# Kernel tuning notes

Hardware: AMD Instinct MI355X
Metric: run time of the kernel (lower is better)

The kernel has to match this reference:

```python
import jax, jax.numpy as jnp
import numpy as np
from jax import lax

V, H, B, S, T = 32000, 512, 32, 256, 16  # vocab, hidden, batch, src_len, keyword_len


def setup_inputs() -> dict:
    key = jax.random.key(0)
    ks = jax.random.split(key, 26)
    sc = 0.02
    def P(k, *shape):
        return jax.random.normal(k, shape, jnp.float32) * sc
    return {
        "theme": jax.random.randint(ks[0], (1, B), 0, V),
        "keyword": jax.random.randint(ks[1], (T, B), 0, V),
        "src": jax.random.randint(ks[2], (S, B), 0, V),
        "theme_tab": P(ks[3], V, H),
        "keyword_tab": P(ks[4], V, H),
        "src_tab": P(ks[5], V, H),
        # GRU params (PyTorch layout: W_ih/W_hh are (3H, H) stacked r,z,n)
        "Wih_f": P(ks[6], 3 * H, H), "Whh_f": P(ks[7], 3 * H, H),
        "bih_f": P(ks[8], 3 * H), "bhh_f": P(ks[9], 3 * H),
        "Wih_b": P(ks[10], 3 * H, H), "Whh_b": P(ks[11], 3 * H, H),
        "bih_b": P(ks[12], 3 * H), "bhh_b": P(ks[13], 3 * H),
        # Linear layers (PyTorch layout: W is (out, in))
        "Ww": P(ks[14], H, 2 * H), "bw": P(ks[15], H),      # enc_w_weight
        "Wt": P(ks[16], H, H), "bt": P(ks[17], H),          # enc_theme_weight
        "Wk": P(ks[18], H, H), "bk": P(ks[19], H),          # enc_keyword_weight
        "wv": P(ks[20], H), "bv": P(ks[21]),                # enc_weight (H -> 1)
        "Wo": P(ks[22], H, 3 * H), "bo": P(ks[23], H),      # enc_output_out
        "Who": P(ks[24], H, 2 * H),                         # enc_hidden_out (no bias)
    }


def _gru_dir(x, Wih, Whh, bih, bhh, reverse):
    # x: (S, B, H). Returns (outputs (S,B,H), final hidden (B,H)).
    h = Whh.shape[1]
    gx = jnp.einsum('sbh,gh->sbg', x, Wih) + bih  # precompute input gates for all steps
    if reverse:
        gx = gx[::-1]
    h0 = jnp.zeros((x.shape[1], h), x.dtype)

    def step(hprev, g):
        gh = hprev @ Whh.T + bhh
        xr, xz, xn = jnp.split(g, 3, axis=-1)
        hr, hz, hn = jnp.split(gh, 3, axis=-1)
        r = jax.nn.sigmoid(xr + hr)
        z = jax.nn.sigmoid(xz + hz)
        n = jnp.tanh(xn + r * hn)
        hnew = (1.0 - z) * n + z * hprev
        return hnew, hnew

    hT, ys = lax.scan(step, h0, gx)
    if reverse:
        ys = ys[::-1]
    return ys, hT


def _forward(theme, keyword, src,
             theme_tab, keyword_tab, src_tab,
             Wih_f, Whh_f, bih_f, bhh_f,
             Wih_b, Whh_b, bih_b, bhh_b,
             Ww, bw, Wt, bt, Wk, bk, wv, bv, Wo, bo, Who):
    hdim = Whh_f.shape[1]
    src_emb = src_tab[src]          # (S, B, H)
    theme_emb = theme_tab[theme]    # (1, B, H)
    keyword_emb = keyword_tab[keyword]  # (T, B, H)

    ys_f, hT_f = _gru_dir(src_emb, Wih_f, Whh_f, bih_f, bhh_f, reverse=False)
    ys_b, hT_b = _gru_dir(src_emb, Wih_b, Whh_b, bih_b, bhh_b, reverse=True)
    enc_output = jnp.concatenate([ys_f, ys_b], axis=-1)   # (S, B, 2H); == enc_w_1 (the split/cat is identity)
    enc_hidden = jnp.concatenate([hT_f, hT_b], axis=-1)[None]  # (1, B, 2H)

    enc_w_1 = enc_output.transpose(1, 0, 2)     # (B, S, 2H)
    enc_theme = theme_emb.transpose(1, 0, 2)    # (B, 1, H)
    enc_keyword = keyword_emb.transpose(1, 0, 2)  # (B, T, H)

    # point(): additive-attention broadcast scoring
    b1 = enc_w_1 @ Ww.T + bw                    # (B, S, H)
    theme_proj = enc_theme[:, 0, :] @ Wt.T + bt  # (B, H)  == b22
    b3 = enc_keyword @ Wk.T + bk                # (B, T, H)
    b4 = jnp.tanh(b1[:, :, None, :] + theme_proj[:, None, None, :] + b3[:, None, :, :])  # (B,S,T,H)
    scores = b4 @ wv + bv                        # (B, S, T)
    enc_w_2 = jnp.einsum('bst,bh->bsh', scores, theme_proj)  # bmm(scores, b22 broadcast over T)

    concat_enc_w = jnp.concatenate([enc_w_2, enc_w_1], axis=-1)  # (B, S, 3H)
    enc_out = (concat_enc_w @ Wo.T + bo).transpose(1, 0, 2)      # (S, B, H)
    enc_hidden_out = enc_hidden @ Who.T                          # (1, B, H)
    return enc_out, enc_hidden_out


def reference(theme, keyword, src,
              theme_tab, keyword_tab, src_tab,
              Wih_f, Whh_f, bih_f, bhh_f,
              Wih_b, Whh_b, bih_b, bhh_b,
              Ww, bw, Wt, bt, Wk, bk, wv, bv, Wo, bo, Who):
    return _forward(theme, keyword, src,
                    theme_tab, keyword_tab, src_tab,
                    Wih_f, Whh_f, bih_f, bhh_f,
                    Wih_b, Whh_b, bih_b, bhh_b,
                    Ww, bw, Wt, bt, Wk, bk, wv, bv, Wo, bo, Who)
```

## Files before the change

### kernel.cpp

```cpp
#include <hip/hip_runtime.h>

typedef unsigned short u16;
typedef __attribute__((ext_vector_type(8))) short bf16x8;
typedef __attribute__((ext_vector_type(4))) float f32x4;

__device__ __forceinline__ float bf2f(u16 u) {
  union { unsigned int i; float f; } v; v.i = ((unsigned int)u) << 16; return v.f;
}
__device__ __forceinline__ u16 f2bf(float f) {
  union { float f; unsigned int i; } v; v.f = f;
  unsigned int r = (v.i + 0x7FFFu + ((v.i >> 16) & 1u)) >> 16;
  return (u16)r;
}
__device__ __forceinline__ float sigmoidf_(float x) { return 1.f / (1.f + __expf(-x)); }
__device__ __forceinline__ float tanhf_(float x) {
  x = fminf(fmaxf(x, -10.f), 10.f);
  float e2 = __expf(2.f * x);
  return (e2 - 1.f) / (e2 + 1.f);
}

static const size_t OFF_GX    = 0;
static const size_t OFF_HBUF  = 50331648;
static const size_t OFF_ASRC  = 67174400;
static const size_t OFF_EW1   = 75563008;
static const size_t OFF_B1    = 92340224;
static const size_t OFF_WIHC  = 109117440;
static const size_t OFF_WWB   = 112263168;
static const size_t OFF_WO2B  = 113311744;
static const size_t OFF_WKB   = 114360320;
static const size_t OFF_KWE   = 114884608;
static const size_t OFF_B3    = 115408896;
static const size_t OFF_TP    = 116457472;
static const size_t OFF_TPO   = 116523008;
static const size_t OFF_SSUM  = 116588544;
static const size_t OFF_BIASC = 116621312;
static const size_t OFF_CNT   = 116633600;

__global__ __launch_bounds__(256) void cvtk(const float* __restrict__ s,
                                            u16* __restrict__ d, int n) {
  int i = (blockIdx.x * 256 + threadIdx.x) * 4;
  if (i < n) {
    float4 v = *(const float4*)(s + i);
    ushort4 o; o.x = f2bf(v.x); o.y = f2bf(v.y); o.z = f2bf(v.z); o.w = f2bf(v.w);
    *(ushort4*)(d + i) = o;
  }
}

__global__ __launch_bounds__(256) void cvt_wo2(const float* __restrict__ Wo,
                                               u16* __restrict__ d) {
  int i = (blockIdx.x * 256 + threadIdx.x) * 4;
  int nrow = i >> 10, c = i & 1023;
  float4 v = *(const float4*)(Wo + (size_t)nrow * 1536 + 512 + c);
  ushort4 o; o.x = f2bf(v.x); o.y = f2bf(v.y); o.z = f2bf(v.z); o.w = f2bf(v.w);
  *(ushort4*)(d + i) = o;
}

__global__ __launch_bounds__(256) void gather_rows(const int* __restrict__ ids,
                                                   const float* __restrict__ tab,
                                                   u16* __restrict__ dst, int mode) {
  int i = (blockIdx.x * 256 + threadIdx.x) * 8;
  int r = i >> 9, c = i & 511;
  int id = (mode == 0) ? ids[r] : ids[((r & 15) << 5) + (r >> 4)];
  const float* s = tab + (size_t)id * 512 + c;
  alignas(16) u16 o[8];
#pragma unroll
  for (int j = 0; j < 8; ++j) o[j] = f2bf(s[j]);
  *(uint4*)(dst + i) = *(const uint4*)o;
}

__global__ __launch_bounds__(256) void proj_tp(const int* __restrict__ theme,
                                               const float* __restrict__ tab,
                                               const float* __restrict__ W,
                                               const float* __restrict__ bias,
                                               float* __restrict__ outp) {
  int o = blockIdx.x * 256 + threadIdx.x;
  int b = o >> 9, n = o & 511;
  const float* emb = tab + (size_t)theme[b] * 512;
  const float* wr = W + (size_t)n * 512;
  float acc = 0.f;
  for (int h = 0; h < 512; h += 4) {
    float4 e = *(const float4*)(emb + h);
    float4 w = *(const float4*)(wr + h);
    acc += e.x * w.x + e.y * w.y + e.z * w.z + e.w * w.w;
  }
  outp[o] = acc + bias[n];
}

__global__ __launch_bounds__(256) void proj_tpo(const float* __restrict__ tp,
                                                const float* __restrict__ Wo,
                                                float* __restrict__ outp) {
  int o = blockIdx.x * 256 + threadIdx.x;
  int b = o >> 9, n = o & 511;
  const float* emb = tp + (size_t)b * 512;
  const float* wr = Wo + (size_t)n * 1536;
  float acc = 0.f;
  for (int h = 0; h < 512; h += 4) {
    float4 e = *(const float4*)(emb + h);
    float4 w = *(const float4*)(wr + h);
    acc += e.x * w.x + e.y * w.y + e.z * w.z + e.w * w.w;
  }
  outp[o] = acc;
}

template <int EPI>
__global__ __launch_bounds__(256) void gemm_bt(const u16* __restrict__ A,
                                               const u16* __restrict__ B,
                                               const float* __restrict__ bias,
                                               float* __restrict__ Cf,
                                               u16* __restrict__ Cb, int M, int N,
                                               int K, const float* __restrict__ ssum,
                                               const float* __restrict__ tpo) {
  __shared__ u16 As[128][72];
  __shared__ u16 Bs[128][72];
  const int tid = threadIdx.x;
  const int mtiles = M >> 7;
  const int mt = blockIdx.x % mtiles, nt = blockIdx.x / mtiles;
  const int wave = tid >> 6, lane = tid & 63;
  const int wr = wave >> 1, wc = wave & 1;
  const int l16 = lane & 15, l4 = lane >> 4;
  f32x4 acc[4][4] = {};
  const int nkt = K >> 6;
  for (int kt = 0; kt < nkt; ++kt) {
    __syncthreads();
#pragma unroll
    for (int i = 0; i < 4; ++i) {
      int c = i * 256 + tid;
      int row = c >> 3, c8 = c & 7;
      uint4 va = *(const uint4*)(A + (size_t)(mt * 128 + row) * K + kt * 64 + c8 * 8);
      *(uint4*)&As[row][c8 * 8] = va;
      uint4 vb = *(const uint4*)(B + (size_t)(nt * 128 + row) * K + kt * 64 + c8 * 8);
      *(uint4*)&Bs[row][c8 * 8] = vb;
    }
    __syncthreads();
#pragma unroll
    for (int kk = 0; kk < 2; ++kk) {
      bf16x8 af[4], bfr[4];
#pragma unroll
      for (int m = 0; m < 4; ++m)
        af[m] = *(const bf16x8*)&As[wr * 64 + m * 16 + l16][kk * 32 + l4 * 8];
#pragma unroll
      for (int n = 0; n < 4; ++n)
        bfr[n] = *(const bf16x8*)&Bs[wc * 64 + n * 16 + l16][kk * 32 + l4 * 8];
#pragma unroll
      for (int m = 0; m < 4; ++m)
#pragma unroll
        for (int n = 0; n < 4; ++n)
          acc[m][n] = __builtin_amdgcn_mfma_f32_16x16x32_bf16(af[m], bfr[n],
                                                              acc[m][n], 0, 0, 0);
    }
  }
#pragma unroll
  for (int m = 0; m < 4; ++m) {
    int rg = mt * 128 + wr * 64 + m * 16 + l4 * 4;
#pragma unroll
    for (int n = 0; n < 4; ++n) {
      int cg = nt * 128 + wc * 64 + n * 16 + l16;
      float bb = bias[cg];
#pragma unroll
      for (int i = 0; i < 4; ++i) {
        int r = rg + i;
        float v = acc[m][n][i] + bb;
        if (EPI == 2) v += ssum[r] * tpo[(r & 31) * 512 + cg];
        if (EPI == 0) Cb[(size_t)r * N + cg] = f2bf(v);
        else Cf[(size_t)r * N + cg] = v;
      }
    }
  }
}

__global__ __launch_bounds__(256) void gru_scan(const u16* __restrict__ gx,
                                                const float* __restrict__ Whh_f,
                                                const float* __restrict__ Whh_b,
                                                const float* __restrict__ bhh_f,
                                                const float* __restrict__ bhh_b,
                                                u16* __restrict__ hbuf,
                                                int* __restrict__ cnt)
{
  __shared__ u16 Wl[96][520];
  __shared__ u16 hl[32 * 512];
  __shared__ float gh[32][100];
  __shared__ float hF[32][32];
  __shared__ float bhs[96];
  const int tid = threadIdx.x;
  const int bid = blockIdx.x;
  const int r8 = bid & 7;
  const int d = r8 >> 2;
  const int slice = (bid >> 3) * 4 + (r8 & 3);
  const float* Whh = d ? Whh_b : Whh_f;
  const float* bhh = d ? bhh_b : bhh_f;

  for (int e = tid * 4; e < 96 * 512; e += 1024) {
    int lr = e >> 9, c = e & 511;
    int grow = (lr >> 5) * 512 + slice * 32 + (lr & 31);
    float4 v = *(const float4*)(Whh + (size_t)grow * 512 + c);
    ushort4 o; o.x = f2bf(v.x); o.y = f2bf(v.y); o.z = f2bf(v.z); o.w = f2bf(v.w);
    *(ushort4*)&Wl[lr][c] = o;
  }
  if (tid < 96) {
    int grow = (tid >> 5) * 512 + slice * 32 + (tid & 31);
    bhs[tid] = bhh[grow];
  }
  for (int e = tid; e < 32 * 32; e += 256) hF[e >> 5][e & 31] = 0.f;

  const int wave = tid >> 6, lane = tid & 63;
  const int l16 = lane & 15, l4 = lane >> 4;
  const int mt = wave & 1, nt3 = (wave >> 1) * 3;
  const int arow = mt * 16 + l16;
  const int asw = (arow & 7) << 4;
  int* cntd = cnt + d * 257;

  __syncthreads();

  for (int t = 0; t < 256; ++t) {
    int trow = (d == 0) ? t : 255 - t;
    const u16* gxr = gx + (size_t)trow * 32 * 3072 + d * 1536 + slice * 32;
    float xr[4], xz[4], xn[4];
#pragma unroll
    for (int it = 0; it < 4; ++it) {
      int item = it * 256 + tid;
      int b = item >> 5, j = item & 31;
      const u16* gxb = gxr + (size_t)b * 3072;
      xr[it] = bf2f(gxb[j]);
      xz[it] = bf2f(gxb[512 + j]);
      xn[it] = bf2f(gxb[1024 + j]);
    }
    if (t > 0) {
      if (tid == 0) {
        while (__hip_atomic_load(cntd + t, __ATOMIC_ACQUIRE,
                                 __HIP_MEMORY_SCOPE_AGENT) < 16)
          __builtin_amdgcn_s_sleep(1);
      }
      __syncthreads();
    }
    const u16* hsrc = hbuf + ((size_t)(d * 257 + t) * 32) * 512;
#pragma unroll
    for (int i = 0; i < 8; ++i) {
      int idx = i * 256 + tid;
      int row = idx >> 6, cb = idx & 63;
      uint4 v = *(const uint4*)(hsrc + row * 512 + cb * 8);
      *(uint4*)((char*)hl + row * 1024 + ((cb * 16) ^ ((row & 7) << 4))) = v;
    }
    __syncthreads();
    f32x4 a0 = {}, a1 = {}, a2 = {};
    const char* hlb = (const char*)hl;
#pragma unroll
    for (int k = 0; k < 16; ++k) {
      int abyte = arow * 1024 + (((k * 32 + l4 * 8) * 2) ^ asw);
      bf16x8 av = *(const bf16x8*)(hlb + abyte);
      bf16x8 b0 = *(const bf16x8*)&Wl[(nt3 + 0) * 16 + l16][k * 32 + l4 * 8];
      bf16x8 b1v = *(const bf16x8*)&Wl[(nt3 + 1) * 16 + l16][k * 32 + l4 * 8];
      bf16x8 b2 = *(const bf16x8*)&Wl[(nt3 + 2) * 16 + l16][k * 32 + l4 * 8];
      a0 = __builtin_amdgcn_mfma_f32_16x16x32_bf16(av, b0, a0, 0, 0, 0);
      a1 = __builtin_amdgcn_mfma_f32_16x16x32_bf16(av, b1v, a1, 0, 0, 0);
      a2 = __builtin_amdgcn_mfma_f32_16x16x32_bf16(av, b2, a2, 0, 0, 0);
    }
    {
      int crow = mt * 16 + l4 * 4;
#pragma unroll
      for (int i = 0; i < 4; ++i) {
        gh[crow + i][(nt3 + 0) * 16 + l16] = a0[i];
        gh[crow + i][(nt3 + 1) * 16 + l16] = a1[i];
        gh[crow + i][(nt3 + 2) * 16 + l16] = a2[i];
      }
    }
    __syncthreads();
    u16* hdst = hbuf + ((size_t)(d * 257 + t + 1) * 32) * 512 + slice * 32;
#pragma unroll
    for (int it = 0; it < 4; ++it) {
      int item = it * 256 + tid;
      int b = item >> 5, j = item & 31;
      float hr = gh[b][j] + bhs[j];
      float hz = gh[b][32 + j] + bhs[32 + j];
      float hn = gh[b][64 + j] + bhs[64 + j];
      float rr = sigmoidf_(xr[it] + hr);
      float zz = sigmoidf_(xz[it] + hz);
      float nn = tanhf_(xn[it] + rr * hn);
      float hp = hF[b][j];
      float hnew = (1.f - zz) * nn + zz * hp;
      hF[b][j] = hnew;
      hdst[(size_t)b * 512 + j] = f2bf(hnew);
    }
    __syncthreads();
    if (tid == 0)
      __hip_atomic_fetch_add(cntd + t + 1, 1, __ATOMIC_RELEASE,
                             __HIP_MEMORY_SCOPE_AGENT);
  }
}

__global__ __launch_bounds__(256) void build_encw1(const u16* __restrict__ hbuf,
                                                   u16* __restrict__ ew) {
  int idx = (blockIdx.x * 256 + threadIdx.x) * 8;
  int r = idx >> 10, c = idx & 1023;
  int s = r >> 5, b = r & 31;
  size_t src;
  if (c < 512) src = ((size_t)(s + 1) * 32 + b) * 512 + c;
  else src = ((size_t)(257 + 256 - s) * 32 + b) * 512 + (c - 512);
  *(uint4*)(ew + idx) = *(const uint4*)(hbuf + src);
}

__global__ __launch_bounds__(256) void scores_k(const float* __restrict__ b1,
                                                const float* __restrict__ tp,
                                                const float* __restrict__ b3,
                                                const float* __restrict__ wv,
                                                const float* __restrict__ bv,
                                                float* __restrict__ ssum) {
  __shared__ float pre[512];
  __shared__ float wvs[512];
  __shared__ float red[4];
  int r = blockIdx.x;
  int tid = threadIdx.x;
  int b = r & 31;
  for (int h = tid; h < 512; h += 256) {
    pre[h] = b1[(size_t)r * 512 + h] + tp[b * 512 + h];
    wvs[h] = wv[h];
  }
  __syncthreads();
  float acc = 0.f;
  for (int t = 0; t < 16; ++t) {
    const float* b3r = b3 + ((size_t)b * 16 + t) * 512;
    for (int h = tid; h < 512; h += 256) acc += wvs[h] * tanhf_(pre[h] + b3r[h]);
  }
  for (int o = 32; o > 0; o >>= 1) acc += __shfl_down(acc, o);
  if ((tid & 63) == 0) red[tid >> 6] = acc;
  __syncthreads();
  if (tid == 0) ssum[r] = red[0] + red[1] + red[2] + red[3] + 16.f * bv[0];
}

__global__ __launch_bounds__(256) void hidden_k(const u16* __restrict__ hbuf,
                                                const float* __restrict__ Who,
                                                float* __restrict__ outp) {
  int o = blockIdx.x * 256 + threadIdx.x;
  int b = o >> 9, n = o & 511;
  const u16* hf = hbuf + ((size_t)256 * 32 + b) * 512;
  const u16* hb = hbuf + ((size_t)(257 + 256) * 32 + b) * 512;
  const float* w = Who + (size_t)n * 1024;
  float acc = 0.f;
  for (int k = 0; k < 512; ++k) acc += bf2f(hf[k]) * w[k];
  for (int k = 0; k < 512; ++k) acc += bf2f(hb[k]) * w[512 + k];
  outp[o] = acc;
}

extern "C" void kernel_launch(void* const* d_in, const int* in_sizes, int n_in,
                              void* d_out, int out_size, void* d_ws, size_t ws_size,
                              hipStream_t stream) {
  (void)in_sizes; (void)n_in; (void)out_size; (void)ws_size;
  const int* theme = (const int*)d_in[0];
  const int* keyword = (const int*)d_in[1];
  const int* src = (const int*)d_in[2];
  const float* theme_tab = (const float*)d_in[3];
  const float* keyword_tab = (const float*)d_in[4];
  const float* src_tab = (const float*)d_in[5];
  const float* Wih_f = (const float*)d_in[6];
  const float* Whh_f = (const float*)d_in[7];
  const float* bih_f = (const float*)d_in[8];
  const float* bhh_f = (const float*)d_in[9];
  const float* Wih_b = (const float*)d_in[10];
  const float* Whh_b = (const float*)d_in[11];
  const float* bih_b = (const float*)d_in[12];
  const float* bhh_b = (const float*)d_in[13];
  const float* Ww = (const float*)d_in[14];
  const float* bw = (const float*)d_in[15];
  const float* Wt = (const float*)d_in[16];
  const float* bt = (const float*)d_in[17];
  const float* Wk = (const float*)d_in[18];
  const float* bk = (const float*)d_in[19];
  const float* wv = (const float*)d_in[20];
  const float* bv = (const float*)d_in[21];
  const float* Wo = (const float*)d_in[22];
  const float* bo = (const float*)d_in[23];
  const float* Who = (const float*)d_in[24];
  float* out = (float*)d_out;
  char* ws = (char*)d_ws;

  u16* gx_cat = (u16*)(ws + OFF_GX);
  u16* hbuf = (u16*)(ws + OFF_HBUF);
  u16* asrc = (u16*)(ws + OFF_ASRC);
  u16* ew1 = (u16*)(ws + OFF_EW1);
  float* b1buf = (float*)(ws + OFF_B1);
  u16* wihc = (u16*)(ws + OFF_WIHC);
  u16* wwb = (u16*)(ws + OFF_WWB);
  u16* wo2b = (u16*)(ws + OFF_WO2B);
  u16* wkb = (u16*)(ws + OFF_WKB);
  u16* kwe = (u16*)(ws + OFF_KWE);
  float* b3buf = (float*)(ws + OFF_B3);
  float* tp = (float*)(ws + OFF_TP);
  float* tpo = (float*)(ws + OFF_TPO);
  float* ssum = (float*)(ws + OFF_SSUM);
  float* biasc = (float*)(ws + OFF_BIASC);
  int* cnt = (int*)(ws + OFF_CNT);

  hipMemsetAsync(cnt, 0, 2 * 257 * 4, stream);
  hipMemsetAsync(hbuf, 0, 32 * 512 * 2, stream);
  hipMemsetAsync(hbuf + (size_t)257 * 32 * 512, 0, 32 * 512 * 2, stream);
  hipMemcpyAsync(biasc, bih_f, 1536 * 4, hipMemcpyDeviceToDevice, stream);
  hipMemcpyAsync(biasc + 1536, bih_b, 1536 * 4, hipMemcpyDeviceToDevice, stream);

  cvtk<<<768, 256, 0, stream>>>(Wih_f, wihc, 1536 * 512);
  cvtk<<<768, 256, 0, stream>>>(Wih_b, wihc + 1536 * 512, 1536 * 512);
  cvtk<<<512, 256, 0, stream>>>(Ww, wwb, 512 * 1024);
  cvtk<<<256, 256, 0, stream>>>(Wk, wkb, 512 * 512);
  cvt_wo2<<<512, 256, 0, stream>>>(Wo, wo2b);
  gather_rows<<<2048, 256, 0, stream>>>(src, src_tab, asrc, 0);
  gather_rows<<<128, 256, 0, stream>>>(keyword, keyword_tab, kwe, 1);
  proj_tp<<<64, 256, 0, stream>>>(theme, theme_tab, Wt, bt, tp);
  proj_tpo<<<64, 256, 0, stream>>>(tp, Wo, tpo);
  gemm_bt<1><<<16, 256, 0, stream>>>(kwe, wkb, bk, b3buf, nullptr, 512, 512, 512,
                                     nullptr, nullptr);
  gemm_bt<0><<<1536, 256, 0, stream>>>(asrc, wihc, biasc, nullptr, gx_cat, 8192,
                                       3072, 512, nullptr, nullptr);
  gru_scan<<<32, 256, 0, stream>>>(gx_cat, Whh_f, Whh_b, bhh_f, bhh_b, hbuf, cnt);
  build_encw1<<<4096, 256, 0, stream>>>(hbuf, ew1);
  gemm_bt<1><<<256, 256, 0, stream>>>(ew1, wwb, bw, b1buf, nullptr, 8192, 512, 1024,
                                      nullptr, nullptr);
  scores_k<<<8192, 256, 0, stream>>>(b1buf, tp, b3buf, wv, bv, ssum);
  gemm_bt<2><<<256, 256, 0, stream>>>(ew1, wo2b, bo, out, nullptr, 8192, 512, 1024,
                                      ssum, tpo);
  hidden_k<<<64, 256, 0, stream>>>(hbuf, Who, out + 4194304);
}
```

Before: 1.399 ms.

## Restructure GRU scan with register-resident weights and per-wave flag synchronization

The persistent GRU scan kernel now keeps its slice of Whh in registers as bf16 MFMA fragments instead of LDS. It uses 512 threads and splits the K dimension across two wave halves, which reduce partial sums through a small LDS buffer. The single per-step counter with a tid-0 spin and block barrier is replaced by per-wave flags polled by a whole wave. Hidden state is read directly from global memory with relaxed atomic loads instead of being staged into LDS. This targets the per-step latency of the serial recurrence, at the cost of heavy register pressure and more fine-grained memory-ordering logic that must stay correct.

```diff
diff --git a/kernel.cpp b/kernel.cpp
--- a/kernel.cpp
+++ b/kernel.cpp
@@ -1,6 +1,7 @@
 #include <hip/hip_runtime.h>
 
 typedef unsigned short u16;
+typedef unsigned long long u64;
 typedef __attribute__((ext_vector_type(8))) short bf16x8;
 typedef __attribute__((ext_vector_type(4))) float f32x4;
 
@@ -34,7 +35,7 @@
 static const size_t OFF_TPO   = 116523008;
 static const size_t OFF_SSUM  = 116588544;
 static const size_t OFF_BIASC = 116621312;
-static const size_t OFF_CNT   = 116633600;
+static const size_t OFF_FLG   = 116633600;
 
 __global__ __launch_bounds__(256) void cvtk(const float* __restrict__ s,
                                             u16* __restrict__ d, int n) {
@@ -168,122 +169,125 @@
   }
 }
 
-__global__ __launch_bounds__(256) void gru_scan(const u16* __restrict__ gx,
-                                                const float* __restrict__ Whh_f,
-                                                const float* __restrict__ Whh_b,
-                                                const float* __restrict__ bhh_f,
-                                                const float* __restrict__ bhh_b,
-                                                u16* __restrict__ hbuf,
-                                                int* __restrict__ cnt)
+__global__ __launch_bounds__(512, 1) void gru_scan(
+    const u16* __restrict__ gx,
+    const float* __restrict__ Whh_f, const float* __restrict__ Whh_b,
+    const float* __restrict__ bhh_f, const float* __restrict__ bhh_b,
+    u16* __restrict__ hbuf,
+    int* __restrict__ flg)
 {
-  __shared__ u16 Wl[96][520];
-  __shared__ u16 hl[32 * 512];
-  __shared__ float gh[32][100];
-  __shared__ float hF[32][32];
-  __shared__ float bhs[96];
+  __shared__ float pbuf[4][3][4][64];
   const int tid = threadIdx.x;
   const int bid = blockIdx.x;
-  const int r8 = bid & 7;
-  const int d = r8 >> 2;
-  const int slice = (bid >> 3) * 4 + (r8 & 3);
+  const int d = bid & 1;
+  const int slice = bid >> 1;
   const float* Whh = d ? Whh_b : Whh_f;
   const float* bhh = d ? bhh_b : bhh_f;
 
-  for (int e = tid * 4; e < 96 * 512; e += 1024) {
-    int lr = e >> 9, c = e & 511;
-    int grow = (lr >> 5) * 512 + slice * 32 + (lr & 31);
-    float4 v = *(const float4*)(Whh + (size_t)grow * 512 + c);
-    ushort4 o; o.x = f2bf(v.x); o.y = f2bf(v.y); o.z = f2bf(v.z); o.w = f2bf(v.w);
-    *(ushort4*)&Wl[lr][c] = o;
-  }
-  if (tid < 96) {
-    int grow = (tid >> 5) * 512 + slice * 32 + (tid & 31);
-    bhs[tid] = bhh[grow];
-  }
-  for (int e = tid; e < 32 * 32; e += 256) hF[e >> 5][e & 31] = 0.f;
-
   const int wave = tid >> 6, lane = tid & 63;
+  const int kh = wave >> 2, m = (wave >> 1) & 1, a = wave & 1;
+  const int p = m * 2 + a;
   const int l16 = lane & 15, l4 = lane >> 4;
-  const int mt = wave & 1, nt3 = (wave >> 1) * 3;
-  const int arow = mt * 16 + l16;
-  const int asw = (arow & 7) << 4;
-  int* cntd = cnt + d * 257;
-
-  __syncthreads();
+  const int j = a * 16 + l16;
+
+  bf16x8 wfrag[3][8];
+#pragma unroll
+  for (int g = 0; g < 3; ++g) {
+    const float* wrow = Whh + (size_t)(g * 512 + slice * 32 + j) * 512;
+#pragma unroll
+    for (int kk = 0; kk < 8; ++kk) {
+      const float* wp = wrow + (kh * 8 + kk) * 32 + l4 * 8;
+      float4 v0 = *(const float4*)wp;
+      float4 v1 = *(const float4*)(wp + 4);
+      alignas(16) u16 tmp[8];
+      tmp[0] = f2bf(v0.x); tmp[1] = f2bf(v0.y); tmp[2] = f2bf(v0.z); tmp[3] = f2bf(v0.w);
+      tmp[4] = f2bf(v1.x); tmp[5] = f2bf(v1.y); tmp[6] = f2bf(v1.z); tmp[7] = f2bf(v1.w);
+      wfrag[g][kk] = *(const bf16x8*)tmp;
+    }
+  }
+  float bR = 0.f, bZ = 0.f, bN = 0.f;
+  if (kh == 0) {
+    bR = bhh[slice * 32 + j];
+    bZ = bhh[512 + slice * 32 + j];
+    bN = bhh[1024 + slice * 32 + j];
+  }
+  float hreg[4] = {0.f, 0.f, 0.f, 0.f};
+
+  const size_t dbase = (size_t)d * 257 * 32 * 512;
+  int* const flgd = flg + (size_t)d * 257 * 64;
 
   for (int t = 0; t < 256; ++t) {
-    int trow = (d == 0) ? t : 255 - t;
-    const u16* gxr = gx + (size_t)trow * 32 * 3072 + d * 1536 + slice * 32;
-    float xr[4], xz[4], xn[4];
-#pragma unroll
-    for (int it = 0; it < 4; ++it) {
-      int item = it * 256 + tid;
-      int b = item >> 5, j = item & 31;
-      const u16* gxb = gxr + (size_t)b * 3072;
-      xr[it] = bf2f(gxb[j]);
-      xz[it] = bf2f(gxb[512 + j]);
-      xn[it] = bf2f(gxb[1024 + j]);
-    }
+    float xg[3][4];
+    if (kh == 0) {
+      int trow = d ? (255 - t) : t;
+      const u16* gb = gx + (size_t)(trow * 32 + m * 16 + l4 * 4) * 3072 +
+                      d * 1536 + slice * 32 + j;
+#pragma unroll
+      for (int i = 0; i < 4; ++i)
+#pragma unroll
+        for (int g = 0; g < 3; ++g)
+          xg[g][i] = bf2f(gb[(size_t)i * 3072 + g * 512]);
+      __builtin_amdgcn_sched_barrier(0);
+    }
+
     if (t > 0) {
-      if (tid == 0) {
-        while (__hip_atomic_load(cntd + t, __ATOMIC_ACQUIRE,
-                                 __HIP_MEMORY_SCOPE_AGENT) < 16)
-          __builtin_amdgcn_s_sleep(1);
+      const int* fp = flgd + (size_t)t * 64 + lane;
+      while (true) {
+        int v = __hip_atomic_load(fp, __ATOMIC_RELAXED, __HIP_MEMORY_SCOPE_AGENT);
+        if (__all(v != 0)) break;
+        __builtin_amdgcn_s_sleep(1);
       }
-      __syncthreads();
-    }
-    const u16* hsrc = hbuf + ((size_t)(d * 257 + t) * 32) * 512;
-#pragma unroll
-    for (int i = 0; i < 8; ++i) {
-      int idx = i * 256 + tid;
-      int row = idx >> 6, cb = idx & 63;
-      uint4 v = *(const uint4*)(hsrc + row * 512 + cb * 8);
-      *(uint4*)((char*)hl + row * 1024 + ((cb * 16) ^ ((row & 7) << 4))) = v;
+      __builtin_amdgcn_fence(__ATOMIC_ACQUIRE, "agent");
+    }
+
+    const u16* hsrc = hbuf + dbase + (size_t)t * 32 * 512;
+    u64 alo[8], ahi[8];
+#pragma unroll
+    for (int kk = 0; kk < 8; ++kk) {
+      const u64* ap = (const u64*)(hsrc + (size_t)(m * 16 + l16) * 512 +
+                                   (kh * 8 + kk) * 32 + l4 * 8);
+      alo[kk] = __hip_atomic_load(ap, __ATOMIC_RELAXED, __HIP_MEMORY_SCOPE_AGENT);
+      ahi[kk] = __hip_atomic_load(ap + 1, __ATOMIC_RELAXED, __HIP_MEMORY_SCOPE_AGENT);
+    }
+
+    f32x4 acc[3] = {};
+#pragma unroll
+    for (int kk = 0; kk < 8; ++kk) {
+      union { u64 u[2]; bf16x8 v; } cv;
+      cv.u[0] = alo[kk]; cv.u[1] = ahi[kk];
+#pragma unroll
+      for (int g = 0; g < 3; ++g)
+        acc[g] = __builtin_amdgcn_mfma_f32_16x16x32_bf16(cv.v, wfrag[g][kk],
+                                                         acc[g], 0, 0, 0);
+    }
+
+    if (kh == 1) {
+#pragma unroll
+      for (int g = 0; g < 3; ++g)
+#pragma unroll
+        for (int i = 0; i < 4; ++i) pbuf[p][g][i][lane] = acc[g][i];
     }
     __syncthreads();
-    f32x4 a0 = {}, a1 = {}, a2 = {};
-    const char* hlb = (const char*)hl;
-#pragma unroll
-    for (int k = 0; k < 16; ++k) {
-      int abyte = arow * 1024 + (((k * 32 + l4 * 8) * 2) ^ asw);
-      bf16x8 av = *(const bf16x8*)(hlb + abyte);
-      bf16x8 b0 = *(const bf16x8*)&Wl[(nt3 + 0) * 16 + l16][k * 32 + l4 * 8];
-      bf16x8 b1v = *(const bf16x8*)&Wl[(nt3 + 1) * 16 + l16][k * 32 + l4 * 8];
-      bf16x8 b2 = *(const bf16x8*)&Wl[(nt3 + 2) * 16 + l16][k * 32 + l4 * 8];
-      a0 = __builtin_amdgcn_mfma_f32_16x16x32_bf16(av, b0, a0, 0, 0, 0);
-      a1 = __builtin_amdgcn_mfma_f32_16x16x32_bf16(av, b1v, a1, 0, 0, 0);
-      a2 = __builtin_amdgcn_mfma_f32_16x16x32_bf16(av, b2, a2, 0, 0, 0);
-    }
-    {
-      int crow = mt * 16 + l4 * 4;
+
+    if (kh == 0) {
+      u16* hdst = hbuf + dbase + (size_t)(t + 1) * 32 * 512 + slice * 32 + j;
 #pragma unroll
       for (int i = 0; i < 4; ++i) {
-        gh[crow + i][(nt3 + 0) * 16 + l16] = a0[i];
-        gh[crow + i][(nt3 + 1) * 16 + l16] = a1[i];
-        gh[crow + i][(nt3 + 2) * 16 + l16] = a2[i];
+        float hr = acc[0][i] + pbuf[p][0][i][lane] + bR;
+        float hz = acc[1][i] + pbuf[p][1][i][lane] + bZ;
+        float hn = acc[2][i] + pbuf[p][2][i][lane] + bN;
+        float rr = sigmoidf_(xg[0][i] + hr);
+        float zz = sigmoidf_(xg[1][i] + hz);
+        float nn = tanhf_(xg[2][i] + rr * hn);
+        hreg[i] = (1.f - zz) * nn + zz * hreg[i];
+        __hip_atomic_store((u16*)(hdst + (size_t)(m * 16 + l4 * 4 + i) * 512),
+                           f2bf(hreg[i]), __ATOMIC_RELAXED, __HIP_MEMORY_SCOPE_AGENT);
       }
-    }
-    __syncthreads();
-    u16* hdst = hbuf + ((size_t)(d * 257 + t + 1) * 32) * 512 + slice * 32;
-#pragma unroll
-    for (int it = 0; it < 4; ++it) {
-      int item = it * 256 + tid;
-      int b = item >> 5, j = item & 31;
-      float hr = gh[b][j] + bhs[j];
-      float hz = gh[b][32 + j] + bhs[32 + j];
-      float hn = gh[b][64 + j] + bhs[64 + j];
-      float rr = sigmoidf_(xr[it] + hr);
-      float zz = sigmoidf_(xz[it] + hz);
-      float nn = tanhf_(xn[it] + rr * hn);
-      float hp = hF[b][j];
-      float hnew = (1.f - zz) * nn + zz * hp;
-      hF[b][j] = hnew;
-      hdst[(size_t)b * 512 + j] = f2bf(hnew);
-    }
-    __syncthreads();
-    if (tid == 0)
-      __hip_atomic_fetch_add(cntd + t + 1, 1, __ATOMIC_RELEASE,
-                             __HIP_MEMORY_SCOPE_AGENT);
+      __builtin_amdgcn_fence(__ATOMIC_RELEASE, "agent");
+      if (lane == 0)
+        __hip_atomic_store(flgd + (size_t)(t + 1) * 64 + slice * 4 + p, 1,
+                           __ATOMIC_RELAXED, __HIP_MEMORY_SCOPE_AGENT);
+    }
   }
 }
 
@@ -387,9 +391,9 @@
   float* tpo = (float*)(ws + OFF_TPO);
   float* ssum = (float*)(ws + OFF_SSUM);
   float* biasc = (float*)(ws + OFF_BIASC);
-  int* cnt = (int*)(ws + OFF_CNT);
-
-  hipMemsetAsync(cnt, 0, 2 * 257 * 4, stream);
+  int* flg = (int*)(ws + OFF_FLG);
+
+  hipMemsetAsync(flg, 0, 2 * 257 * 64 * 4, stream);
   hipMemsetAsync(hbuf, 0, 32 * 512 * 2, stream);
   hipMemsetAsync(hbuf + (size_t)257 * 32 * 512, 0, 32 * 512 * 2, stream);
   hipMemcpyAsync(biasc, bih_f, 1536 * 4, hipMemcpyDeviceToDevice, stream);
@@ -408,7 +412,7 @@
                                      nullptr, nullptr);
   gemm_bt<0><<<1536, 256, 0, stream>>>(asrc, wihc, biasc, nullptr, gx_cat, 8192,
                                        3072, 512, nullptr, nullptr);
-  gru_scan<<<32, 256, 0, stream>>>(gx_cat, Whh_f, Whh_b, bhh_f, bhh_b, hbuf, cnt);
+  gru_scan<<<32, 512, 0, stream>>>(gx_cat, Whh_f, Whh_b, bhh_f, bhh_b, hbuf, flg);
   build_encw1<<<4096, 256, 0, stream>>>(hbuf, ew1);
   gemm_bt<1><<<256, 256, 0, stream>>>(ew1, wwb, bw, b1buf, nullptr, 8192, 512, 1024,
                                       nullptr, nullptr);
```

Measured after the change: 2.617 ms. +87.1%, slower.

## Replace GRU step counter atomics with per-block flags and swizzle Whh LDS

Applied to the files above, without the earlier changes.

Cross-block step synchronization in the GRU scan switches from one atomic counter per step, which 16 blocks increment and one thread polls, to a per-block flag array. A whole wave polls the 16 flags with relaxed loads plus `__all`, then issues an acquire fence. Producers wait on vmcnt, issue a release fence and do a plain store. The Whh tile in LDS also changes from padded rows to an XOR-swizzled layout to avoid bank conflicts, and the block-to-(direction, slice) mapping changes. The aim is lower per-step synchronization latency in the serial 256-step recurrence, at the cost of correctness depending on the hand-written fence/waitcnt ordering.

```diff
diff --git a/kernel.cpp b/kernel.cpp
--- a/kernel.cpp
+++ b/kernel.cpp
@@ -1,6 +1,7 @@
 #include <hip/hip_runtime.h>
 
 typedef unsigned short u16;
+typedef unsigned long long u64;
 typedef __attribute__((ext_vector_type(8))) short bf16x8;
 typedef __attribute__((ext_vector_type(4))) float f32x4;
 
@@ -34,7 +35,7 @@
 static const size_t OFF_TPO   = 116523008;
 static const size_t OFF_SSUM  = 116588544;
 static const size_t OFF_BIASC = 116621312;
-static const size_t OFF_CNT   = 116633600;
+static const size_t OFF_FLG   = 116633600;
 
 __global__ __launch_bounds__(256) void cvtk(const float* __restrict__ s,
                                             u16* __restrict__ d, int n) {
@@ -168,24 +169,22 @@
   }
 }
 
-__global__ __launch_bounds__(256) void gru_scan(const u16* __restrict__ gx,
-                                                const float* __restrict__ Whh_f,
-                                                const float* __restrict__ Whh_b,
-                                                const float* __restrict__ bhh_f,
-                                                const float* __restrict__ bhh_b,
-                                                u16* __restrict__ hbuf,
-                                                int* __restrict__ cnt)
+__global__ __launch_bounds__(256) void gru_scan(
+    const u16* __restrict__ gx,
+    const float* __restrict__ Whh_f, const float* __restrict__ Whh_b,
+    const float* __restrict__ bhh_f, const float* __restrict__ bhh_b,
+    u16* __restrict__ hbuf,
+    int* __restrict__ flg)
 {
-  __shared__ u16 Wl[96][520];
+  __shared__ u16 Wl[96 * 512];
   __shared__ u16 hl[32 * 512];
   __shared__ float gh[32][100];
   __shared__ float hF[32][32];
   __shared__ float bhs[96];
   const int tid = threadIdx.x;
   const int bid = blockIdx.x;
-  const int r8 = bid & 7;
-  const int d = r8 >> 2;
-  const int slice = (bid >> 3) * 4 + (r8 & 3);
+  const int d = bid & 1;
+  const int slice = bid >> 1;
   const float* Whh = d ? Whh_b : Whh_f;
   const float* bhh = d ? bhh_b : bhh_f;
 
@@ -194,7 +193,7 @@
     int grow = (lr >> 5) * 512 + slice * 32 + (lr & 31);
     float4 v = *(const float4*)(Whh + (size_t)grow * 512 + c);
     ushort4 o; o.x = f2bf(v.x); o.y = f2bf(v.y); o.z = f2bf(v.z); o.w = f2bf(v.w);
-    *(ushort4*)&Wl[lr][c] = o;
+    *(ushort4*)((char*)Wl + lr * 1024 + ((c * 2) ^ ((lr & 7) << 4))) = o;
   }
   if (tid < 96) {
     int grow = (tid >> 5) * 512 + slice * 32 + (tid & 31);
@@ -207,7 +206,7 @@
   const int mt = wave & 1, nt3 = (wave >> 1) * 3;
   const int arow = mt * 16 + l16;
   const int asw = (arow & 7) << 4;
-  int* cntd = cnt + d * 257;
+  int* const flgd = flg + (size_t)d * 257 * 16;
 
   __syncthreads();
 
@@ -225,10 +224,14 @@
       xn[it] = bf2f(gxb[1024 + j]);
     }
     if (t > 0) {
-      if (tid == 0) {
-        while (__hip_atomic_load(cntd + t, __ATOMIC_ACQUIRE,
-                                 __HIP_MEMORY_SCOPE_AGENT) < 16)
+      if (wave == 0) {
+        const int* fp = flgd + (size_t)t * 16 + l16;
+        while (true) {
+          int v = __hip_atomic_load(fp, __ATOMIC_RELAXED, __HIP_MEMORY_SCOPE_AGENT);
+          if (__all(v != 0)) break;
           __builtin_amdgcn_s_sleep(1);
+        }
+        __builtin_amdgcn_fence(__ATOMIC_ACQUIRE, "agent");
       }
       __syncthreads();
     }
@@ -243,13 +246,17 @@
     __syncthreads();
     f32x4 a0 = {}, a1 = {}, a2 = {};
     const char* hlb = (const char*)hl;
+    const char* wlb = (const char*)Wl;
+    const int r0 = (nt3 + 0) * 16 + l16, s0 = (r0 & 7) << 4;
+    const int r1 = (nt3 + 1) * 16 + l16, s1 = (r1 & 7) << 4;
+    const int r2 = (nt3 + 2) * 16 + l16, s2 = (r2 & 7) << 4;
 #pragma unroll
     for (int k = 0; k < 16; ++k) {
-      int abyte = arow * 1024 + (((k * 32 + l4 * 8) * 2) ^ asw);
-      bf16x8 av = *(const bf16x8*)(hlb + abyte);
-      bf16x8 b0 = *(const bf16x8*)&Wl[(nt3 + 0) * 16 + l16][k * 32 + l4 * 8];
-      bf16x8 b1v = *(const bf16x8*)&Wl[(nt3 + 1) * 16 + l16][k * 32 + l4 * 8];
-      bf16x8 b2 = *(const bf16x8*)&Wl[(nt3 + 2) * 16 + l16][k * 32 + l4 * 8];
+      int cb = (k * 32 + l4 * 8) * 2;
+      bf16x8 av = *(const bf16x8*)(hlb + arow * 1024 + (cb ^ asw));
+      bf16x8 b0 = *(const bf16x8*)(wlb + r0 * 1024 + (cb ^ s0));
+      bf16x8 b1v = *(const bf16x8*)(wlb + r1 * 1024 + (cb ^ s1));
+      bf16x8 b2 = *(const bf16x8*)(wlb + r2 * 1024 + (cb ^ s2));
       a0 = __builtin_amdgcn_mfma_f32_16x16x32_bf16(av, b0, a0, 0, 0, 0);
       a1 = __builtin_amdgcn_mfma_f32_16x16x32_bf16(av, b1v, a1, 0, 0, 0);
       a2 = __builtin_amdgcn_mfma_f32_16x16x32_bf16(av, b2, a2, 0, 0, 0);
@@ -280,10 +287,13 @@
       hF[b][j] = hnew;
       hdst[(size_t)b * 512 + j] = f2bf(hnew);
     }
+    asm volatile("s_waitcnt vmcnt(0)" ::: "memory");
     __syncthreads();
-    if (tid == 0)
-      __hip_atomic_fetch_add(cntd + t + 1, 1, __ATOMIC_RELEASE,
-                             __HIP_MEMORY_SCOPE_AGENT);
+    if (tid == 0) {
+      __builtin_amdgcn_fence(__ATOMIC_RELEASE, "agent");
+      __hip_atomic_store(flgd + (size_t)(t + 1) * 16 + slice, 1,
+                         __ATOMIC_RELAXED, __HIP_MEMORY_SCOPE_AGENT);
+    }
   }
 }
 
@@ -387,9 +397,9 @@
   float* tpo = (float*)(ws + OFF_TPO);
   float* ssum = (float*)(ws + OFF_SSUM);
   float* biasc = (float*)(ws + OFF_BIASC);
-  int* cnt = (int*)(ws + OFF_CNT);
-
-  hipMemsetAsync(cnt, 0, 2 * 257 * 4, stream);
+  int* flg = (int*)(ws + OFF_FLG);
+
+  hipMemsetAsync(flg, 0, 2 * 257 * 16 * 4, stream);
   hipMemsetAsync(hbuf, 0, 32 * 512 * 2, stream);
   hipMemsetAsync(hbuf + (size_t)257 * 32 * 512, 0, 32 * 512 * 2, stream);
   hipMemcpyAsync(biasc, bih_f, 1536 * 4, hipMemcpyDeviceToDevice, stream);
@@ -408,7 +418,7 @@
                                      nullptr, nullptr);
   gemm_bt<0><<<1536, 256, 0, stream>>>(asrc, wihc, biasc, nullptr, gx_cat, 8192,
                                        3072, 512, nullptr, nullptr);
-  gru_scan<<<32, 256, 0, stream>>>(gx_cat, Whh_f, Whh_b, bhh_f, bhh_b, hbuf, cnt);
+  gru_scan<<<32, 256, 0, stream>>>(gx_cat, Whh_f, Whh_b, bhh_f, bhh_b, hbuf, flg);
   build_encw1<<<4096, 256, 0, stream>>>(hbuf, ew1);
   gemm_bt<1><<<256, 256, 0, stream>>>(ew1, wwb, bw, b1buf, nullptr, 8192, 512, 1024,
                                       nullptr, nullptr);
```

After: 1.417 ms. Within noise of the previous version (+1.3%).
